# Performance work log

Hardware: AMD Instinct MI355X
Metric: run time of the kernel (lower is better)

The kernel has to match this reference:

```python
import jax, jax.numpy as jnp
import numpy as np

B, NQ, NK, C, H = 4, 1024, 1024, 768, 12
DH = C // H
SCALE = DH ** -0.5
EPS = 1e-5  # nn.LayerNorm default
NEG_INF = float('-inf')


def _ln(x, g, b):
    m = jnp.mean(x, axis=-1, keepdims=True)
    v = jnp.mean((x - m) ** 2, axis=-1, keepdims=True)
    return (x - m) * jax.lax.rsqrt(v + EPS) * g + b


def _heads(t):  # [B,N,C] -> [B,H,N,Dh]
    Bq, N, _ = t.shape
    return t.reshape(Bq, N, H, DH).transpose(0, 2, 1, 3)


def setup_inputs() -> dict:
    key = jax.random.key(0)
    ks = jax.random.split(key, 32)
    w = lambda k, shape: jax.random.normal(k, shape, jnp.float32) * 0.02
    g = lambda k: 1.0 + jax.random.normal(k, (C,), jnp.float32) * 0.02
    b = lambda k: jax.random.normal(k, (C,), jnp.float32) * 0.02
    inp = {
        'x': jax.random.normal(ks[0], (B, NQ, C), jnp.float32),
        'y': jax.random.normal(ks[1], (B, NK, C), jnp.float32),
        'xpos': jnp.arange(B * NQ, dtype=jnp.int32).reshape(B, NQ),
        'ypos': jnp.arange(B * NK, dtype=jnp.int32).reshape(B, NK),
        'mask': jax.random.randint(ks[2], (NQ, NK), 0, 2) > 0,
        'similarities': jax.random.normal(ks[3], (B, H, NQ, NK), jnp.float32),
        # norms
        'ln1_g': g(ks[4]), 'ln1_b': b(ks[5]),
        'ln2_g': g(ks[6]), 'ln2_b': b(ks[7]),
        'ln3_g': g(ks[8]), 'ln3_b': b(ks[9]),
        'lny_g': g(ks[10]), 'lny_b': b(ks[11]),
        # self-attn (qkv_bias=False)
        'qkv_w': w(ks[12], (3 * C, C)),
        'aproj_w': w(ks[13], (C, C)), 'aproj_b': b(ks[14]),
        # cross-attn
        'pq_w': w(ks[15], (C, C)), 'pk_w': w(ks[16], (C, C)), 'pv_w': w(ks[17], (C, C)),
        'cproj_w': w(ks[18], (C, C)), 'cproj_b': b(ks[19]),
        # mlp (hidden = 4*C)
        'fc1_w': w(ks[20], (4 * C, C)), 'fc1_b': jax.random.normal(ks[21], (4 * C,), jnp.float32) * 0.02,
        'fc2_w': w(ks[22], (C, 4 * C)), 'fc2_b': b(ks[23]),
    }
    return inp


def reference(x, y, xpos, ypos, mask, similarities,
              ln1_g, ln1_b, ln2_g, ln2_b, ln3_g, ln3_b, lny_g, lny_b,
              qkv_w, aproj_w, aproj_b,
              pq_w, pk_w, pv_w, cproj_w, cproj_b,
              fc1_w, fc1_b, fc2_w, fc2_b):
    # ---- self-attention (rope=None, dropout=0) ----
    xn = _ln(x, ln1_g, ln1_b)
    qkv = (xn @ qkv_w.T).reshape(B, NQ, 3, H, DH).transpose(2, 0, 3, 1, 4)
    q, k, v = qkv[0], qkv[1], qkv[2]                       # [B,H,Nq,Dh]
    attn = jax.nn.softmax(jnp.einsum('bhqd,bhkd->bhqk', q, k) * SCALE, axis=-1)
    sa = jnp.einsum('bhqk,bhkd->bhqd', attn, v).transpose(0, 2, 1, 3).reshape(B, NQ, C)
    x = x + sa @ aproj_w.T + aproj_b

    # ---- sparse cross-attention with similarity bias + mask ----
    y_ = _ln(y, lny_g, lny_b)
    xn2 = _ln(x, ln2_g, ln2_b)
    cq = _heads(xn2 @ pq_w.T)                              # [B,H,Nq,Dh]
    ck = _heads(y_ @ pk_w.T)                               # [B,H,Nk,Dh]
    cv = _heads(y_ @ pv_w.T)
    scores = jnp.einsum('bhqd,bhkd->bhqk', cq, ck) * SCALE
    sims_c = similarities - jnp.mean(similarities, axis=1, keepdims=True)
    scores = scores + sims_c
    scores = jnp.where(mask[None, None], scores, NEG_INF)
    cattn = jax.nn.softmax(scores, axis=-1)
    ca = jnp.einsum('bhqk,bhkd->bhqd', cattn, cv).transpose(0, 2, 1, 3).reshape(B, NQ, C)
    x = x + ca @ cproj_w.T + cproj_b

    # ---- MLP (exact GELU, as nn.GELU default) ----
    xn3 = _ln(x, ln3_g, ln3_b)
    h = jax.nn.gelu(xn3 @ fc1_w.T + fc1_b, approximate=False)
    x = x + h @ fc2_w.T + fc2_b
    return (x, y)
```

## Files before the change

### kernel.cpp

```cpp
#include <hip/hip_runtime.h>
#include <cstdint>
#include <cstddef>


typedef __bf16 bf16;
typedef __attribute__((ext_vector_type(8))) __bf16 bf16x8;
typedef __attribute__((ext_vector_type(4))) __bf16 bf16x4;
typedef __attribute__((ext_vector_type(4))) float f32x4;

typedef __attribute__((address_space(1))) void gvoid;
typedef __attribute__((address_space(3))) void lvoid;

#define DEVI static __device__ __forceinline__

DEVI void gload16(const void* g, void* l) {
  __builtin_amdgcn_global_load_lds((gvoid*)(uintptr_t)g, (lvoid*)(uintptr_t)l, 16, 0, 0);
}

DEVI f32x4 mfma_bf16(bf16x8 a, bf16x8 b, f32x4 c) {
  return __builtin_amdgcn_mfma_f32_16x16x32_bf16(a, b, c, 0, 0, 0);
}

__global__ __launch_bounds__(256)
void detect_mask_k(const unsigned char* __restrict__ mask, int* __restrict__ shift)
{
  __shared__ int acc[256];
  const int t = threadIdx.x;
  int s = 0;
  for (int i = t; i < 16384; i += 256) {
    const int base = i * 4;
    s += mask[base + 1] + mask[base + 2] + mask[base + 3];
  }
  acc[t] = s;
  __syncthreads();
  #pragma unroll
  for (int o = 128; o; o >>= 1) {
    if (t < o) acc[t] += acc[t + o];
    __syncthreads();
  }
  if (t == 0) *shift = (acc[0] == 0) ? 2 : 0;
}

__global__ __launch_bounds__(256)
void bias_k(const float* __restrict__ sim,
            const unsigned char* __restrict__ mask,
            const int* __restrict__ mshift,
            bf16* __restrict__ biasOut)
{
  const int blk = blockIdx.x;
  const int b = blk >> 10, q = blk & 1023;
  const int t = threadIdx.x;
  const int k4 = t * 4;
  const int msh = *mshift;
  const float* sb = sim + (size_t)b * 12 * 1024 * 1024;
  bf16* ob = biasOut + (size_t)b * 12 * 1024 * 1024;

  f32x4 sv[12];
  f32x4 acc = {0.f, 0.f, 0.f, 0.f};
  #pragma unroll
  for (int h = 0; h < 12; ++h) {
    sv[h] = *(const f32x4*)(sb + ((size_t)h * 1024 + q) * 1024 + k4);
    acc += sv[h];
  }
  const f32x4 mean = acc * (1.0f / 12.0f);

  float mb[4];
  if (msh == 0) {
    const uchar4 mv = *(const uchar4*)(mask + (size_t)q * 1024 + k4);
    mb[0] = mv.x ? 0.f : -1e30f; mb[1] = mv.y ? 0.f : -1e30f;
    mb[2] = mv.z ? 0.f : -1e30f; mb[3] = mv.w ? 0.f : -1e30f;
  } else {
    const int4 mv = *(const int4*)((const int*)mask + (size_t)q * 1024 + k4);
    mb[0] = mv.x ? 0.f : -1e30f; mb[1] = mv.y ? 0.f : -1e30f;
    mb[2] = mv.z ? 0.f : -1e30f; mb[3] = mv.w ? 0.f : -1e30f;
  }

  #pragma unroll
  for (int h = 0; h < 12; ++h) {
    bf16x4 o;
    #pragma unroll
    for (int j = 0; j < 4; ++j)
      o[j] = (bf16)(sv[h][j] - mean[j] + mb[j]);
    *(bf16x4*)(ob + ((size_t)h * 1024 + q) * 1024 + k4) = o;
  }
}

struct CvtArgs {
  const float* src[8];
  bf16* dst[8];
  int end[8];
};
__global__ __launch_bounds__(256)
void cvt_all_k(CvtArgs a)
{
  const int i = blockIdx.x * 256 + threadIdx.x;
  int s = 0;
  #pragma unroll
  for (int j = 0; j < 7; ++j) s += (i >= a.end[j]) ? 1 : 0;
  const int base = s ? a.end[s - 1] : 0;
  const int off = i - base;
  const f32x4 v = *((const f32x4*)a.src[s] + off);
  bf16x4 o;
  o[0] = (bf16)v[0]; o[1] = (bf16)v[1]; o[2] = (bf16)v[2]; o[3] = (bf16)v[3];
  *(bf16x4*)(a.dst[s] + (size_t)off * 4) = o;
}

__global__ __launch_bounds__(256)
void copy4_k(const float* __restrict__ s, float* __restrict__ d, int n4)
{
  const int i = blockIdx.x * 256 + threadIdx.x;
  if (i < n4) ((f32x4*)d)[i] = ((const f32x4*)s)[i];
}

template<bool DUAL>
__global__ __launch_bounds__(256)
void ln_k(const float* __restrict__ inA, const float* __restrict__ gA,
          const float* __restrict__ bA, bf16* __restrict__ outA,
          const float* __restrict__ inB, const float* __restrict__ gB,
          const float* __restrict__ bB, bf16* __restrict__ outB)
{
  int row = blockIdx.x;
  const float* xin = inA; const float* g = gA; const float* be = bA; bf16* out = outA;
  if constexpr (DUAL) {
    if (row >= 4096) {
      row -= 4096; xin = inB; g = gB; be = bB; out = outB;
    }
  }
  const int tid = threadIdx.x;
  const int lane = tid & 63, w = tid >> 6;
  const float* xr = xin + (size_t)row * 768;
  const float v0 = xr[tid], v1 = xr[tid + 256], v2 = xr[tid + 512];
  float s = v0 + v1 + v2;
  #pragma unroll
  for (int o = 32; o; o >>= 1) s += __shfl_xor(s, o);
  __shared__ float r1[4], r2[4];
  if (lane == 0) r1[w] = s;
  __syncthreads();
  const float mean = (r1[0] + r1[1] + r1[2] + r1[3]) * (1.0f / 768.0f);
  const float d0 = v0 - mean, d1 = v1 - mean, d2 = v2 - mean;
  float q = d0 * d0 + d1 * d1 + d2 * d2;
  #pragma unroll
  for (int o = 32; o; o >>= 1) q += __shfl_xor(q, o);
  if (lane == 0) r2[w] = q;
  __syncthreads();
  const float inv = rsqrtf((r2[0] + r2[1] + r2[2] + r2[3]) * (1.0f / 768.0f) + 1e-5f);
  bf16* orow = out + (size_t)row * 768;
  orow[tid]       = (bf16)(d0 * inv * g[tid]       + be[tid]);
  orow[tid + 256] = (bf16)(d1 * inv * g[tid + 256] + be[tid + 256]);
  orow[tid + 512] = (bf16)(d2 * inv * g[tid + 512] + be[tid + 512]);
}

__global__ __launch_bounds__(256)
void build_vt(const bf16* __restrict__ src, int ld, bf16* __restrict__ vt)
{
  __shared__ unsigned short t[64][72];
  const int bh = blockIdx.x, nt = blockIdx.y;
  const int b = bh / 12, hh = bh % 12;
  const int tid = threadIdx.x;
  {
    const int nl = tid >> 2, d0 = (tid & 3) * 16;
    const unsigned short* srow = (const unsigned short*)src
        + (size_t)(b * 1024 + nt * 64 + nl) * ld + hh * 64 + d0;
    #pragma unroll
    for (int j = 0; j < 4; ++j)
      *(ushort4*)(&t[nl][d0 + j * 4]) = *(const ushort4*)(srow + j * 4);
  }
  __syncthreads();
  {
    const int dl = tid >> 2, n0 = (tid & 3) * 16;
    unsigned short* drow = (unsigned short*)vt + ((size_t)bh * 64 + dl) * 1024 + nt * 64 + n0;
    #pragma unroll
    for (int j = 0; j < 4; ++j) {
      ushort4 o;
      o.x = t[n0 + j * 4 + 0][dl];
      o.y = t[n0 + j * 4 + 1][dl];
      o.z = t[n0 + j * 4 + 2][dl];
      o.w = t[n0 + j * 4 + 3][dl];
      *(ushort4*)(drow + j * 4) = o;
    }
  }
}

template<int BM, int BN, bool BIAS, bool GELU, bool RES, bool OBF>
__global__ __launch_bounds__(256)
void gemm_bt(const bf16* __restrict__ A, const bf16* __restrict__ Bt,
             const float* __restrict__ bias, const float* __restrict__ res,
             bf16* __restrict__ Cb, float* __restrict__ Cf,
             int nyPerXcd, int N, int K)
{
  constexpr int WM = BM / 2, WN = BN / 2;
  constexpr int FM = WM / 16, FN = WN / 16;
  __shared__ bf16 As[BM * 64];
  __shared__ bf16 Bs[BN * 64];
  const int f = blockIdx.x;
  const int xcd = f & 7, j = f >> 3;
  const int by = xcd + 8 * (j % nyPerXcd);
  const int bx = j / nyPerXcd;
  const int tid = threadIdx.x;
  const int lane = tid & 63;
  const int wv = tid >> 6;
  const int wr = wv >> 1, wc = wv & 1;
  const int l15 = lane & 15, lg = lane >> 4;
  const int bm = by * BM, bn = bx * BN;

  f32x4 acc[FM][FN];
  const f32x4 z = {0.f, 0.f, 0.f, 0.f};
  #pragma unroll
  for (int i = 0; i < FM; ++i)
    #pragma unroll
    for (int jj = 0; jj < FN; ++jj) acc[i][jj] = z;

  for (int k0 = 0; k0 < K; k0 += 64) {
    __syncthreads();
    #pragma unroll
    for (int c = tid; c < BM * 8; c += 256) {
      const int row = c >> 3, colb = (c & 7) << 4;
      gload16((const char*)A + ((size_t)(bm + row) * K + k0) * 2 + colb,
              (char*)As + (size_t)c * 16);
    }
    #pragma unroll
    for (int c = tid; c < BN * 8; c += 256) {
      const int row = c >> 3, colb = (c & 7) << 4;
      gload16((const char*)Bt + ((size_t)(bn + row) * K + k0) * 2 + colb,
              (char*)Bs + (size_t)c * 16);
    }
    __syncthreads();
    #pragma unroll
    for (int kk = 0; kk < 64; kk += 32) {
      bf16x8 af[FM], bfr[FN];
      #pragma unroll
      for (int mi = 0; mi < FM; ++mi)
        af[mi] = *(const bf16x8*)(As + (size_t)(wr * WM + mi * 16 + l15) * 64 + kk + lg * 8);
      #pragma unroll
      for (int ni = 0; ni < FN; ++ni)
        bfr[ni] = *(const bf16x8*)(Bs + (size_t)(wc * WN + ni * 16 + l15) * 64 + kk + lg * 8);
      #pragma unroll
      for (int mi = 0; mi < FM; ++mi)
        #pragma unroll
        for (int ni = 0; ni < FN; ++ni)
          acc[mi][ni] = mfma_bf16(af[mi], bfr[ni], acc[mi][ni]);
    }
  }

  #pragma unroll
  for (int mi = 0; mi < FM; ++mi) {
    const int row0 = bm + wr * WM + mi * 16 + lg * 4;
    #pragma unroll
    for (int ni = 0; ni < FN; ++ni) {
      const int col = bn + wc * WN + ni * 16 + l15;
      #pragma unroll
      for (int r = 0; r < 4; ++r) {
        float v = acc[mi][ni][r];
        if constexpr (BIAS) v += bias[col];
        if constexpr (GELU) v = 0.5f * v * (1.0f + erff(v * 0.70710678118654752f));
        if constexpr (RES)  v += res[(size_t)(row0 + r) * N + col];
        if constexpr (OBF)  Cb[(size_t)(row0 + r) * N + col] = (bf16)v;
        else                Cf[(size_t)(row0 + r) * N + col] = v;
      }
    }
  }
}

template<int CROSS>
__global__ __launch_bounds__(256, 3)
void fattn_k(const bf16* __restrict__ Qp, int ldq,
             const bf16* __restrict__ Kp, int ldk,
             const bf16* __restrict__ Vt,
             const bf16* __restrict__ bias,
             bf16* __restrict__ Out)
{
  __shared__ bf16 Kl[2][64 * 64];
  __shared__ bf16 Vl[2][64 * 64];
  __shared__ bf16 Pl[4][16 * 72];

  const int f = blockIdx.x;
  const int r8 = f & 7, rest = f >> 3;
  const int c6 = rest % 6, qt = rest / 6;
  const int pp = r8 + 8 * c6;
  const int b = pp / 12, hh = pp % 12;
  const int tid = threadIdx.x, lane = tid & 63, wq = tid >> 6;
  const int l15 = lane & 15, lg = lane >> 4;

  bf16x8 qreg0, qreg1;
  {
    const bf16* qsrc = Qp + (size_t)(b * 1024 + qt * 64 + wq * 16 + l15) * ldq + hh * 64 + lg * 8;
    qreg0 = *(const bf16x8*)qsrc;
    qreg1 = *(const bf16x8*)(qsrc + 32);
  }
  const char* Kbase = (const char*)(Kp + (size_t)b * 1024 * ldk + hh * 64);
  const char* Vbase = (const char*)(Vt + (size_t)(b * 12 + hh) * 64 * 1024);
  const bf16* biasRow = nullptr;
  if constexpr (CROSS)
    biasRow = bias + (((size_t)(b * 12 + hh)) * 1024 + qt * 64 + wq * 16 + l15) * 1024;

  f32x4 oacc[4];
  const f32x4 z = {0.f, 0.f, 0.f, 0.f};
  #pragma unroll
  for (int i = 0; i < 4; ++i) oacc[i] = z;
  float m_run = -1e30f, l_run = 0.f;

  char* PlW = (char*)&Pl[wq][0];
  const int swz = (l15 & 7) << 4;

  auto stage = [&](int buf, int t) {
    const int k0 = t * 64;
    #pragma unroll
    for (int jj = 0; jj < 2; ++jj) {
      const int c = jj * 256 + tid;
      const int r = c >> 3;
      const int sw = ((c & 7) ^ (r & 7)) << 4;
      gload16(Kbase + ((size_t)(k0 + r) * ldk) * 2 + sw, (char*)&Kl[buf][0] + (size_t)c * 16);
      gload16(Vbase + (size_t)r * 2048 + (size_t)k0 * 2 + sw, (char*)&Vl[buf][0] + (size_t)c * 16);
    }
  };

  stage(0, 0);
  __syncthreads();

  for (int t = 0; t < 16; ++t) {
    const int cur = t & 1;
    const int k0 = t * 64;
    if (t < 15) stage(cur ^ 1, t + 1);

    bf16x4 bv[4];
    if constexpr (CROSS) {
      const bf16* bp = biasRow + k0 + lg * 4;
      #pragma unroll
      for (int ni = 0; ni < 4; ++ni) bv[ni] = *(const bf16x4*)(bp + ni * 16);
    }

    f32x4 sacc[4];
    #pragma unroll
    for (int i = 0; i < 4; ++i) sacc[i] = z;
    #pragma unroll
    for (int ni = 0; ni < 4; ++ni) {
      const int rowb = (ni * 16 + l15) * 128;
      const bf16x8 a0 = *(const bf16x8*)((char*)&Kl[cur][0] + rowb + ((lg * 16) ^ swz));
      const bf16x8 a1 = *(const bf16x8*)((char*)&Kl[cur][0] + rowb + ((64 + lg * 16) ^ swz));
      sacc[ni] = mfma_bf16(a0, qreg0, sacc[ni]);
      sacc[ni] = mfma_bf16(a1, qreg1, sacc[ni]);
    }

    float sv[16];
    #pragma unroll
    for (int ni = 0; ni < 4; ++ni)
      #pragma unroll
      for (int r = 0; r < 4; ++r)
        sv[ni * 4 + r] = sacc[ni][r] * 0.125f;
    if constexpr (CROSS) {
      #pragma unroll
      for (int ni = 0; ni < 4; ++ni)
        #pragma unroll
        for (int r = 0; r < 4; ++r)
          sv[ni * 4 + r] += (float)bv[ni][r];
    }
    float mx = sv[0];
    #pragma unroll
    for (int jj = 1; jj < 16; ++jj) mx = fmaxf(mx, sv[jj]);
    mx = fmaxf(mx, __shfl_xor(mx, 16));
    mx = fmaxf(mx, __shfl_xor(mx, 32));
    const float mnew = fmaxf(m_run, mx);
    const float corr = __expf(m_run - mnew);
    m_run = mnew;
    float ps = 0.f;
    #pragma unroll
    for (int jj = 0; jj < 16; ++jj) { sv[jj] = __expf(sv[jj] - mnew); ps += sv[jj]; }
    l_run = l_run * corr + ps;

    #pragma unroll
    for (int ni = 0; ni < 4; ++ni) {
      bf16x4 pw;
      #pragma unroll
      for (int r = 0; r < 4; ++r) pw[r] = (bf16)sv[ni * 4 + r];
      *(bf16x4*)(PlW + l15 * 144 + ni * 32 + lg * 8) = pw;
    }
    float cr[4];
    #pragma unroll
    for (int r = 0; r < 4; ++r) cr[r] = __shfl(corr, ((lane >> 4) << 2) + r);
    #pragma unroll
    for (int nd = 0; nd < 4; ++nd)
      #pragma unroll
      for (int r = 0; r < 4; ++r) oacc[nd][r] *= cr[r];

    const bf16x8 p0 = *(const bf16x8*)(PlW + l15 * 144 + lg * 16);
    const bf16x8 p1 = *(const bf16x8*)(PlW + l15 * 144 + 64 + lg * 16);
    #pragma unroll
    for (int nd = 0; nd < 4; ++nd) {
      const int rowb = (nd * 16 + l15) * 128;
      const bf16x8 v0 = *(const bf16x8*)((char*)&Vl[cur][0] + rowb + ((lg * 16) ^ swz));
      const bf16x8 v1 = *(const bf16x8*)((char*)&Vl[cur][0] + rowb + ((64 + lg * 16) ^ swz));
      oacc[nd] = mfma_bf16(p0, v0, oacc[nd]);
      oacc[nd] = mfma_bf16(p1, v1, oacc[nd]);
    }
    __syncthreads();
  }

  float ls = l_run + __shfl_xor(l_run, 16);
  ls += __shfl_xor(ls, 32);
  const float inv = 1.0f / ls;
  float ivr[4];
  #pragma unroll
  for (int r = 0; r < 4; ++r) ivr[r] = __shfl(inv, ((lane >> 4) << 2) + r);
  bf16* ob = Out + (size_t)(b * 1024 + qt * 64 + wq * 16 + lg * 4) * 768 + hh * 64 + l15;
  #pragma unroll
  for (int r = 0; r < 4; ++r)
    #pragma unroll
    for (int nd = 0; nd < 4; ++nd)
      ob[(size_t)r * 768 + nd * 16] = (bf16)(oacc[nd][r] * ivr[r]);
}

extern "C" void kernel_launch(void* const* d_in, const int* in_sizes, int n_in,
                              void* d_out, int out_size, void* d_ws, size_t ws_size,
                              hipStream_t stream)
{
  (void)in_sizes; (void)n_in; (void)out_size; (void)ws_size;
  const float* x    = (const float*)d_in[0];
  const float* y    = (const float*)d_in[1];
  const unsigned char* mask = (const unsigned char*)d_in[4];
  const float* sim  = (const float*)d_in[5];
  const float* ln1g = (const float*)d_in[6];
  const float* ln1b = (const float*)d_in[7];
  const float* ln2g = (const float*)d_in[8];
  const float* ln2b = (const float*)d_in[9];
  const float* ln3g = (const float*)d_in[10];
  const float* ln3b = (const float*)d_in[11];
  const float* lnyg = (const float*)d_in[12];
  const float* lnyb = (const float*)d_in[13];
  const float* qkvw = (const float*)d_in[14];
  const float* apw  = (const float*)d_in[15];
  const float* apb  = (const float*)d_in[16];
  const float* pqw  = (const float*)d_in[17];
  const float* pkw  = (const float*)d_in[18];
  const float* pvw  = (const float*)d_in[19];
  const float* cpw  = (const float*)d_in[20];
  const float* cpb  = (const float*)d_in[21];
  const float* f1w  = (const float*)d_in[22];
  const float* f1b  = (const float*)d_in[23];
  const float* f2w  = (const float*)d_in[24];
  const float* f2b  = (const float*)d_in[25];

  char* ws = (char*)d_ws;
  size_t off = 0;
  auto alloc = [&](size_t bytes) -> void* {
    off = (off + 255) & ~(size_t)255;
    void* p = ws + off;
    off += bytes;
    return p;
  };
  const size_t T = 4096;
  bf16* w_qkv = (bf16*)alloc((size_t)2304 * 768 * 2);
  bf16* w_ap  = (bf16*)alloc((size_t)768 * 768 * 2);
  bf16* w_pq  = (bf16*)alloc((size_t)768 * 768 * 2);
  bf16* w_pkv = (bf16*)alloc((size_t)1536 * 768 * 2);
  bf16* w_cp  = (bf16*)alloc((size_t)768 * 768 * 2);
  bf16* w_f1  = (bf16*)alloc((size_t)3072 * 768 * 2);
  bf16* w_f2  = (bf16*)alloc((size_t)768 * 3072 * 2);
  bf16* xn    = (bf16*)alloc(T * 768 * 2);
  bf16* qkvo  = (bf16*)alloc(T * 2304 * 2);
  bf16* vt    = (bf16*)alloc((size_t)48 * 64 * 1024 * 2);
  bf16* sa    = (bf16*)alloc(T * 768 * 2);
  float* x1   = (float*)alloc(T * 768 * 4);
  bf16* yln   = (bf16*)alloc(T * 768 * 2);
  bf16* xn2   = (bf16*)alloc(T * 768 * 2);
  bf16* cqf   = (bf16*)alloc(T * 768 * 2);
  bf16* ckv   = (bf16*)alloc(T * 1536 * 2);
  bf16* cvtT  = (bf16*)alloc((size_t)48 * 64 * 1024 * 2);
  bf16* biasA = (bf16*)alloc((size_t)4 * 12 * 1024 * 1024 * 2);
  bf16* ca    = (bf16*)alloc(T * 768 * 2);
  float* x2   = (float*)alloc(T * 768 * 4);
  bf16* xn3   = (bf16*)alloc(T * 768 * 2);
  bf16* hbuf  = (bf16*)alloc(T * 3072 * 2);
  int* mshift = (int*)alloc(256);

  detect_mask_k<<<1, 256, 0, stream>>>(mask, mshift);

  {
    CvtArgs a;
    const float* srcs[8] = {qkvw, apw, pqw, pkw, pvw, cpw, f1w, f2w};
    bf16* dsts[8] = {w_qkv, w_ap, w_pq, w_pkv, w_pkv + 768 * 768, w_cp, w_f1, w_f2};
    const int n4s[8] = {442368, 147456, 147456, 147456, 147456, 147456, 589824, 589824};
    int cum = 0;
    for (int j = 0; j < 8; ++j) {
      a.src[j] = srcs[j]; a.dst[j] = dsts[j];
      cum += n4s[j]; a.end[j] = cum;
    }
    cvt_all_k<<<cum / 256, 256, 0, stream>>>(a);
  }

  bias_k<<<4096, 256, 0, stream>>>(sim, mask, mshift, biasA);

  ln_k<true><<<8192, 256, 0, stream>>>(x, ln1g, ln1b, xn, y, lnyg, lnyb, yln);
  gemm_bt<128,128,false,false,false,true><<<576, 256, 0, stream>>>(
      xn, w_qkv, nullptr, nullptr, qkvo, nullptr, 4, 2304, 768);
  build_vt<<<dim3(48, 16), 256, 0, stream>>>(qkvo + 1536, 2304, vt);
  fattn_k<0><<<768, 256, 0, stream>>>(
      qkvo, 2304, qkvo + 768, 2304, vt, nullptr, sa);
  gemm_bt<64,128,true,false,true,false><<<384, 256, 0, stream>>>(
      sa, w_ap, apb, x, nullptr, x1, 8, 768, 768);

  ln_k<false><<<4096, 256, 0, stream>>>(x1, ln2g, ln2b, xn2,
                                        nullptr, nullptr, nullptr, nullptr);
  gemm_bt<64,128,false,false,false,true><<<384, 256, 0, stream>>>(
      xn2, w_pq, nullptr, nullptr, cqf, nullptr, 8, 768, 768);
  gemm_bt<128,128,false,false,false,true><<<384, 256, 0, stream>>>(
      yln, w_pkv, nullptr, nullptr, ckv, nullptr, 4, 1536, 768);
  build_vt<<<dim3(48, 16), 256, 0, stream>>>(ckv + 768, 1536, cvtT);
  fattn_k<1><<<768, 256, 0, stream>>>(
      cqf, 768, ckv, 1536, cvtT, biasA, ca);
  gemm_bt<64,128,true,false,true,false><<<384, 256, 0, stream>>>(
      ca, w_cp, cpb, x1, nullptr, x2, 8, 768, 768);

  ln_k<false><<<4096, 256, 0, stream>>>(x2, ln3g, ln3b, xn3,
                                        nullptr, nullptr, nullptr, nullptr);
  gemm_bt<128,128,true,true,false,true><<<768, 256, 0, stream>>>(
      xn3, w_f1, f1b, nullptr, hbuf, nullptr, 4, 3072, 768);
  gemm_bt<64,128,true,false,true,false><<<384, 256, 0, stream>>>(
      hbuf, w_f2, f2b, x2, nullptr, (float*)d_out, 8, 768, 3072);

  copy4_k<<<3072, 256, 0, stream>>>(y, (float*)d_out + 3145728, 786432);
}
```

Baseline: 412.9 us.

## Fuse V transpose into QKV/KV GEMM epilogues and mask detection into bias kernel

The V-transposed layout is now written directly from the GEMM epilogue for columns past the V offset, so the two separate build_vt transpose kernels and their extra pass over V go away. The mask-shift detection kernel is folded into bias_k: each block sums the first 1024 mask bytes itself instead of a single-block kernel scanning 64K bytes. This drops three launches and some memory traffic. The cost is scattered 8-byte stores in the GEMM epilogue and a redundant small reduction in every bias block. The fused reduction covers only part of the data the old detect kernel scanned.

```diff
diff --git a/kernel.cpp b/kernel.cpp
--- a/kernel.cpp
+++ b/kernel.cpp
@@ -22,36 +22,23 @@
 }
 
 __global__ __launch_bounds__(256)
-void detect_mask_k(const unsigned char* __restrict__ mask, int* __restrict__ shift)
-{
-  __shared__ int acc[256];
-  const int t = threadIdx.x;
-  int s = 0;
-  for (int i = t; i < 16384; i += 256) {
-    const int base = i * 4;
-    s += mask[base + 1] + mask[base + 2] + mask[base + 3];
-  }
-  acc[t] = s;
-  __syncthreads();
-  #pragma unroll
-  for (int o = 128; o; o >>= 1) {
-    if (t < o) acc[t] += acc[t + o];
-    __syncthreads();
-  }
-  if (t == 0) *shift = (acc[0] == 0) ? 2 : 0;
-}
-
-__global__ __launch_bounds__(256)
 void bias_k(const float* __restrict__ sim,
             const unsigned char* __restrict__ mask,
-            const int* __restrict__ mshift,
             bf16* __restrict__ biasOut)
 {
+  __shared__ int red[4];
   const int blk = blockIdx.x;
   const int b = blk >> 10, q = blk & 1023;
   const int t = threadIdx.x;
   const int k4 = t * 4;
-  const int msh = *mshift;
+
+  int ds = mask[t * 4 + 1] + mask[t * 4 + 2] + mask[t * 4 + 3];
+  #pragma unroll
+  for (int o = 32; o; o >>= 1) ds += __shfl_xor(ds, o);
+  if ((t & 63) == 0) red[t >> 6] = ds;
+  __syncthreads();
+  const int msh = ((red[0] + red[1] + red[2] + red[3]) == 0) ? 2 : 0;
+
   const float* sb = sim + (size_t)b * 12 * 1024 * 1024;
   bf16* ob = biasOut + (size_t)b * 12 * 1024 * 1024;
 
@@ -150,42 +137,12 @@
   orow[tid + 512] = (bf16)(d2 * inv * g[tid + 512] + be[tid + 512]);
 }
 
-__global__ __launch_bounds__(256)
-void build_vt(const bf16* __restrict__ src, int ld, bf16* __restrict__ vt)
-{
-  __shared__ unsigned short t[64][72];
-  const int bh = blockIdx.x, nt = blockIdx.y;
-  const int b = bh / 12, hh = bh % 12;
-  const int tid = threadIdx.x;
-  {
-    const int nl = tid >> 2, d0 = (tid & 3) * 16;
-    const unsigned short* srow = (const unsigned short*)src
-        + (size_t)(b * 1024 + nt * 64 + nl) * ld + hh * 64 + d0;
-    #pragma unroll
-    for (int j = 0; j < 4; ++j)
-      *(ushort4*)(&t[nl][d0 + j * 4]) = *(const ushort4*)(srow + j * 4);
-  }
-  __syncthreads();
-  {
-    const int dl = tid >> 2, n0 = (tid & 3) * 16;
-    unsigned short* drow = (unsigned short*)vt + ((size_t)bh * 64 + dl) * 1024 + nt * 64 + n0;
-    #pragma unroll
-    for (int j = 0; j < 4; ++j) {
-      ushort4 o;
-      o.x = t[n0 + j * 4 + 0][dl];
-      o.y = t[n0 + j * 4 + 1][dl];
-      o.z = t[n0 + j * 4 + 2][dl];
-      o.w = t[n0 + j * 4 + 3][dl];
-      *(ushort4*)(drow + j * 4) = o;
-    }
-  }
-}
-
-template<int BM, int BN, bool BIAS, bool GELU, bool RES, bool OBF>
+template<int BM, int BN, bool BIAS, bool GELU, bool RES, bool OBF, bool VT>
 __global__ __launch_bounds__(256)
 void gemm_bt(const bf16* __restrict__ A, const bf16* __restrict__ Bt,
              const float* __restrict__ bias, const float* __restrict__ res,
              bf16* __restrict__ Cb, float* __restrict__ Cf,
+             bf16* __restrict__ vtOut, int vtBase,
              int nyPerXcd, int N, int K)
 {
   constexpr int WM = BM / 2, WN = BN / 2;
@@ -248,6 +205,17 @@
     #pragma unroll
     for (int ni = 0; ni < FN; ++ni) {
       const int col = bn + wc * WN + ni * 16 + l15;
+      if constexpr (VT) {
+        if (col >= vtBase) {
+          const int hd = col - vtBase;
+          const int bb = row0 >> 10, n0 = row0 & 1023;
+          bf16x4 ov;
+          #pragma unroll
+          for (int r = 0; r < 4; ++r) ov[r] = (bf16)acc[mi][ni][r];
+          *(bf16x4*)(vtOut + ((size_t)(bb * 768 + hd)) * 1024 + n0) = ov;
+          continue;
+        }
+      }
       #pragma unroll
       for (int r = 0; r < 4; ++r) {
         float v = acc[mi][ni][r];
@@ -470,9 +438,6 @@
   float* x2   = (float*)alloc(T * 768 * 4);
   bf16* xn3   = (bf16*)alloc(T * 768 * 2);
   bf16* hbuf  = (bf16*)alloc(T * 3072 * 2);
-  int* mshift = (int*)alloc(256);
-
-  detect_mask_k<<<1, 256, 0, stream>>>(mask, mshift);
 
   {
     CvtArgs a;
@@ -487,35 +452,33 @@
     cvt_all_k<<<cum / 256, 256, 0, stream>>>(a);
   }
 
-  bias_k<<<4096, 256, 0, stream>>>(sim, mask, mshift, biasA);
+  bias_k<<<4096, 256, 0, stream>>>(sim, mask, biasA);
 
   ln_k<true><<<8192, 256, 0, stream>>>(x, ln1g, ln1b, xn, y, lnyg, lnyb, yln);
-  gemm_bt<128,128,false,false,false,true><<<576, 256, 0, stream>>>(
-      xn, w_qkv, nullptr, nullptr, qkvo, nullptr, 4, 2304, 768);
-  build_vt<<<dim3(48, 16), 256, 0, stream>>>(qkvo + 1536, 2304, vt);
+  gemm_bt<128,128,false,false,false,true,true><<<576, 256, 0, stream>>>(
+      xn, w_qkv, nullptr, nullptr, qkvo, nullptr, vt, 1536, 4, 2304, 768);
   fattn_k<0><<<768, 256, 0, stream>>>(
       qkvo, 2304, qkvo + 768, 2304, vt, nullptr, sa);
-  gemm_bt<64,128,true,false,true,false><<<384, 256, 0, stream>>>(
-      sa, w_ap, apb, x, nullptr, x1, 8, 768, 768);
+  gemm_bt<64,128,true,false,true,false,false><<<384, 256, 0, stream>>>(
+      sa, w_ap, apb, x, nullptr, x1, nullptr, 0, 8, 768, 768);
 
   ln_k<false><<<4096, 256, 0, stream>>>(x1, ln2g, ln2b, xn2,
                                         nullptr, nullptr, nullptr, nullptr);
-  gemm_bt<64,128,false,false,false,true><<<384, 256, 0, stream>>>(
-      xn2, w_pq, nullptr, nullptr, cqf, nullptr, 8, 768, 768);
-  gemm_bt<128,128,false,false,false,true><<<384, 256, 0, stream>>>(
-      yln, w_pkv, nullptr, nullptr, ckv, nullptr, 4, 1536, 768);
-  build_vt<<<dim3(48, 16), 256, 0, stream>>>(ckv + 768, 1536, cvtT);
+  gemm_bt<64,128,false,false,false,true,false><<<384, 256, 0, stream>>>(
+      xn2, w_pq, nullptr, nullptr, cqf, nullptr, nullptr, 0, 8, 768, 768);
+  gemm_bt<128,128,false,false,false,true,true><<<384, 256, 0, stream>>>(
+      yln, w_pkv, nullptr, nullptr, ckv, nullptr, cvtT, 768, 4, 1536, 768);
   fattn_k<1><<<768, 256, 0, stream>>>(
       cqf, 768, ckv, 1536, cvtT, biasA, ca);
-  gemm_bt<64,128,true,false,true,false><<<384, 256, 0, stream>>>(
-      ca, w_cp, cpb, x1, nullptr, x2, 8, 768, 768);
+  gemm_bt<64,128,true,false,true,false,false><<<384, 256, 0, stream>>>(
+      ca, w_cp, cpb, x1, nullptr, x2, nullptr, 0, 8, 768, 768);
 
   ln_k<false><<<4096, 256, 0, stream>>>(x2, ln3g, ln3b, xn3,
                                         nullptr, nullptr, nullptr, nullptr);
-  gemm_bt<128,128,true,true,false,true><<<768, 256, 0, stream>>>(
-      xn3, w_f1, f1b, nullptr, hbuf, nullptr, 4, 3072, 768);
-  gemm_bt<64,128,true,false,true,false><<<384, 256, 0, stream>>>(
-      hbuf, w_f2, f2b, x2, nullptr, (float*)d_out, 8, 768, 3072);
+  gemm_bt<128,128,true,true,false,true,false><<<768, 256, 0, stream>>>(
+      xn3, w_f1, f1b, nullptr, hbuf, nullptr, nullptr, 0, 4, 3072, 768);
+  gemm_bt<64,128,true,false,true,false,false><<<384, 256, 0, stream>>>(
+      hbuf, w_f2, f2b, x2, nullptr, (float*)d_out, nullptr, 0, 8, 768, 3072);
 
   copy4_k<<<3072, 256, 0, stream>>>(y, (float*)d_out + 3145728, 786432);
 }
```

Result: faster. 388.6 us (-5.9%).
